# Kernel optimization log

Hardware: AMD Instinct MI355X
Metric: run time of the kernel (lower is better)

Reference implementation:

```python
import jax, jax.numpy as jnp
import numpy as np

B, C, N, K, OUT = 4, 192, 10000, 16, 384

def setup_inputs() -> dict:
    key = jax.random.key(0)
    k1, k2, k3, k4 = jax.random.split(key, 4)
    x = jax.random.normal(k1, (B, C, N, 1), dtype=jnp.float32)
    edge_index = jax.random.randint(k2, (2, B, N, K), 0, N, dtype=jnp.int32)
    # 1x1x1 Conv3d weight [OUT, 2C, 1, 1, 1] collapsed to [OUT, 2C]
    fan_in = 2 * C
    weight = jax.random.normal(k3, (OUT, 2 * C), dtype=jnp.float32) / np.sqrt(fan_in)
    bias = jax.random.normal(k4, (OUT,), dtype=jnp.float32) * 0.01
    return {"x": x, "edge_index": edge_index, "weight": weight, "bias": bias}


def _gather_neighbors(x3, idx):
    # x3: [B, C, N], idx: [B, N, K] -> [B, C, N, K]
    return jax.vmap(lambda xb, ib: xb[:, ib])(x3, idx)


def reference(x, edge_index, weight, bias):
    b, c, n, _ = x.shape
    x3 = x[..., 0]                                   # [B, C, N]
    x_i = _gather_neighbors(x3, edge_index[1])       # centers  [B, C, N, K]
    x_j = _gather_neighbors(x3, edge_index[0])       # neighbors [B, C, N, K]
    x_j_max = jnp.max(x_j - x_i, axis=-1)            # max-relative, [B, C, N]
    # torch.cat([x.unsqueeze(2), x_j.unsqueeze(2)], 2).reshape(b, 2c, n, 1)
    # interleaves channels as (x_c, xj_c) pairs
    feat = jnp.stack([x3, x_j_max], axis=2).reshape(b, 2 * c, n)  # [B, 2C, N]
    out = jnp.einsum('oc,bcn->bon', weight, feat) + bias[None, :, None]
    out = jax.nn.relu(out)
    # Conv3d path: output shape [B, OUT, N, 1, 1]
    return out[..., None, None]
```

## Files before the change

### kernel.cpp

```cpp
#include <hip/hip_runtime.h>
#include <hip/hip_bf16.h>


#define NB   4
#define NC   192
#define NN   10000
#define NK   16
#define NOUT 384
#define K2C  384
#define NPAD 10112

typedef short bf16x8 __attribute__((ext_vector_type(8)));
typedef float f32x4  __attribute__((ext_vector_type(4)));

__device__ inline unsigned short f2bf(float f) {
    unsigned int u = __builtin_bit_cast(unsigned int, f);
    u += ((u >> 16) & 1u) + 0x7FFFu;
    return (unsigned short)(u >> 16);
}
__device__ inline float bflo(unsigned int u) {
    return __builtin_bit_cast(float, u << 16);
}
__device__ inline float bfhi(unsigned int u) {
    return __builtin_bit_cast(float, u & 0xFFFF0000u);
}

__global__ __launch_bounds__(256) void k_transpose(const float* __restrict__ x,
                                                   unsigned short* __restrict__ xT) {
    __shared__ unsigned short tile[NC * 65];
    int b  = blockIdx.x & 3;
    int nb = (blockIdx.x >> 2) * 64;
    int t  = threadIdx.x;
    const float* xb = x + (size_t)b * NC * NN;
    for (int i = 0; i < 48; ++i) {
        int idx = i * 256 + t;
        int c  = idx >> 6;
        int nl = idx & 63;
        int n  = nb + nl;
        float v = (n < NN) ? xb[(size_t)c * NN + n] : 0.f;
        tile[c * 65 + nl] = f2bf(v);
    }
    __syncthreads();
    unsigned short* xTb = xT + (size_t)b * NN * NC;
    for (int i = 0; i < 48; ++i) {
        int idx = i * 256 + t;
        int nl  = idx / NC;
        int c   = idx - nl * NC;
        int n   = nb + nl;
        if (n < NN) xTb[(size_t)n * NC + c] = tile[c * 65 + nl];
    }
}

__global__ __launch_bounds__(256) void k_wconv(const float* __restrict__ w,
                                               unsigned short* __restrict__ wbf) {
    int i = blockIdx.x * 256 + threadIdx.x;
    wbf[i] = f2bf(w[i]);
}

__global__ __launch_bounds__(256, 6) void k_gather(const unsigned short* __restrict__ xT,
                                                   const int* __restrict__ eidx,
                                                   unsigned short* __restrict__ featT) {
    int b    = blockIdx.x & 3;
    int tile = blockIdx.x >> 2;
    int wv   = threadIdx.x >> 6;
    int lane = threadIdx.x & 63;
    int lam  = lane & 31;
    int hb   = lane & 32;
    const unsigned int* xr = (const unsigned int*)(xT + (size_t)b * NN * NC);
    unsigned short* fb = featT + (size_t)b * NPAD * K2C;
    int part = lam >> 4;
    const int* ep = eidx + (size_t)part * NB * NN * NK + (size_t)b * NN * NK;

    int nbase = tile * 64 + wv * 16 + (hb ? 8 : 0);

    int v[8];
#pragma unroll
    for (int it = 0; it < 8; ++it) {
        int n = nbase + it;
        v[it] = (n < NN) ? ep[(size_t)n * NK + (lam & 15)] : 0;
    }

    for (int it = 0; it < 8; ++it) {
        int n = nbase + it;
        if (n >= NN) break;
        const unsigned int* crow = xr + (size_t)n * 96;
        unsigned int c0 = crow[lam], c1 = crow[32 + lam], c2 = crow[64 + lam];
        float m0l = -INFINITY, m0h = -INFINITY;
        float m1l = -INFINITY, m1h = -INFINITY;
        float m2l = -INFINITY, m2h = -INFINITY;
#pragma unroll 4
        for (int k = 0; k < 16; ++k) {
            int j = __shfl(v[it], hb + k, 64);
            int i = __shfl(v[it], hb + 16 + k, 64);
            const unsigned int* rj = xr + (size_t)j * 96;
            const unsigned int* ri = xr + (size_t)i * 96;
            unsigned int j0 = rj[lam], j1 = rj[32 + lam], j2 = rj[64 + lam];
            unsigned int i0 = ri[lam], i1 = ri[32 + lam], i2 = ri[64 + lam];
            m0l = fmaxf(m0l, bflo(j0) - bflo(i0));  m0h = fmaxf(m0h, bfhi(j0) - bfhi(i0));
            m1l = fmaxf(m1l, bflo(j1) - bflo(i1));  m1h = fmaxf(m1h, bfhi(j1) - bfhi(i1));
            m2l = fmaxf(m2l, bflo(j2) - bflo(i2));  m2h = fmaxf(m2h, bfhi(j2) - bfhi(i2));
        }
        uint2* orow = (uint2*)(fb + (size_t)n * K2C);
        uint2 o0, o1, o2;
        o0.x = (c0 & 0xFFFFu)  | ((unsigned int)f2bf(m0l) << 16);
        o0.y = (c0 >> 16)      | ((unsigned int)f2bf(m0h) << 16);
        o1.x = (c1 & 0xFFFFu)  | ((unsigned int)f2bf(m1l) << 16);
        o1.y = (c1 >> 16)      | ((unsigned int)f2bf(m1h) << 16);
        o2.x = (c2 & 0xFFFFu)  | ((unsigned int)f2bf(m2l) << 16);
        o2.y = (c2 >> 16)      | ((unsigned int)f2bf(m2h) << 16);
        orow[lam]      = o0;
        orow[32 + lam] = o1;
        orow[64 + lam] = o2;
    }
}

__global__ __launch_bounds__(256, 3) void k_gemm(const unsigned short* __restrict__ wbf,
                                                 const unsigned short* __restrict__ featT,
                                                 const float* __restrict__ bias,
                                                 float* __restrict__ out) {
    __shared__ unsigned short lds[64 * 48 * 8];
    int bid  = blockIdx.x;
    int b    = bid & 3;
    int nt   = bid >> 2;
    int wv   = threadIdx.x >> 6;
    int lane = threadIdx.x & 63;
    int r    = lane & 15;
    int q    = lane >> 4;

    const unsigned short* fbase = featT + (size_t)b * NPAD * K2C + (size_t)(nt * 64) * K2C;
#pragma unroll
    for (int ii = 0; ii < 12; ++ii) {
        int i = wv * 12 + ii;
        unsigned int g = (unsigned int)(i * 64 + lane);
        unsigned int n = g / 48u;
        unsigned int p = g - n * 48u;
        int j = (int)p - (int)((3u * n) % 48u);
        if (j < 0) j += 48;
        const unsigned short* src = fbase + (size_t)n * K2C + (size_t)j * 8;
        __builtin_amdgcn_global_load_lds(
            (const __attribute__((address_space(1))) unsigned int*)src,
            (__attribute__((address_space(3))) unsigned int*)&lds[(size_t)i * 512],
            16, 0, 0);
    }

    const unsigned short* aptr = wbf + (size_t)(wv * 96 + r) * K2C + q * 8;

    unsigned int nbase[4], u0[4];
#pragma unroll
    for (int ni = 0; ni < 4; ++ni) {
        unsigned int n = ni * 16 + r;
        nbase[ni] = n * 48u;
        u0[ni] = ((unsigned int)q + 3u * n) % 48u;
    }

    f32x4 acc[6][4];
#pragma unroll
    for (int mi = 0; mi < 6; ++mi)
#pragma unroll
        for (int ni = 0; ni < 4; ++ni)
            acc[mi][ni] = (f32x4){0.f, 0.f, 0.f, 0.f};

    __syncthreads();

#pragma unroll 2
    for (int t = 0; t < 12; ++t) {
        bf16x8 a[6], bb[4];
#pragma unroll
        for (int mi = 0; mi < 6; ++mi)
            a[mi] = *(const bf16x8*)(aptr + (size_t)mi * 16 * K2C + t * 32);
#pragma unroll
        for (int ni = 0; ni < 4; ++ni) {
            unsigned int u = u0[ni] + 4u * t;
            if (u >= 48u) u -= 48u;
            bb[ni] = *(const bf16x8*)(lds + (size_t)(nbase[ni] + u) * 8);
        }
#pragma unroll
        for (int mi = 0; mi < 6; ++mi)
#pragma unroll
            for (int ni = 0; ni < 4; ++ni)
                acc[mi][ni] = __builtin_amdgcn_mfma_f32_16x16x32_bf16(a[mi], bb[ni], acc[mi][ni], 0, 0, 0);
    }

    float* ob = out + (size_t)b * NOUT * NN;
#pragma unroll
    for (int mi = 0; mi < 6; ++mi) {
        int obase = wv * 96 + mi * 16 + q * 4;
#pragma unroll
        for (int ni = 0; ni < 4; ++ni) {
            int n = nt * 64 + ni * 16 + r;
            if (n < NN) {
#pragma unroll
                for (int rr = 0; rr < 4; ++rr) {
                    int o = obase + rr;
                    float val = acc[mi][ni][rr] + bias[o];
                    ob[(size_t)o * NN + n] = fmaxf(val, 0.f);
                }
            }
        }
    }
}

extern "C" void kernel_launch(void* const* d_in, const int* in_sizes, int n_in,
                              void* d_out, int out_size, void* d_ws, size_t ws_size,
                              hipStream_t stream) {
    const float* x    = (const float*)d_in[0];
    const int*   eidx = (const int*)d_in[1];
    const float* w    = (const float*)d_in[2];
    const float* bias = (const float*)d_in[3];
    float* out = (float*)d_out;

    unsigned short* xT    = (unsigned short*)d_ws;
    unsigned short* featT = xT + (size_t)NB * NN * NC;
    unsigned short* wbf   = featT + (size_t)NB * NPAD * K2C;

    hipLaunchKernelGGL(k_transpose, dim3(4 * 157), dim3(256), 0, stream, x, xT);
    hipLaunchKernelGGL(k_wconv,     dim3(576),     dim3(256), 0, stream, w, wbf);
    hipLaunchKernelGGL(k_gather,    dim3(4 * 157), dim3(256), 0, stream, xT, eidx, featT);
    hipLaunchKernelGGL(k_gemm,      dim3(4 * 158), dim3(256), 0, stream, wbf, featT, bias, out);
}
```

Baseline: 177.7 us.

## Fuse neighbor gather into GEMM via LDS and merge prep kernels

The gather/max-relative stage now writes its bf16 interleaved feature tile directly into LDS in the swizzled layout the MFMA GEMM expects, so the featT intermediate no longer makes a round trip through global memory and one kernel launch is dropped. The transpose and weight conversion are also merged into one launch, with the weight conversion vectorized to float4. The fused kernel runs at the GEMM's lower occupancy (launch bounds 3 instead of 6), so the latency-bound gather phase has fewer waves to hide its random loads. The GEMM phase also cannot start until the whole tile has been gathered.

```diff
diff --git a/kernel.cpp b/kernel.cpp
--- a/kernel.cpp
+++ b/kernel.cpp
@@ -1,5 +1,4 @@
 #include <hip/hip_runtime.h>
-#include <hip/hip_bf16.h>
 
 
 #define NB   4
@@ -8,7 +7,6 @@
 #define NK   16
 #define NOUT 384
 #define K2C  384
-#define NPAD 10112
 
 typedef short bf16x8 __attribute__((ext_vector_type(8)));
 typedef float f32x4  __attribute__((ext_vector_type(4)));
@@ -25,11 +23,23 @@
     return __builtin_bit_cast(float, u & 0xFFFF0000u);
 }
 
-__global__ __launch_bounds__(256) void k_transpose(const float* __restrict__ x,
-                                                   unsigned short* __restrict__ xT) {
+__global__ __launch_bounds__(256) void k_prep(const float* __restrict__ x,
+                                              unsigned short* __restrict__ xT,
+                                              const float* __restrict__ w,
+                                              unsigned short* __restrict__ wbf) {
     __shared__ unsigned short tile[NC * 65];
-    int b  = blockIdx.x & 3;
-    int nb = (blockIdx.x >> 2) * 64;
+    int bid = blockIdx.x;
+    if (bid >= 628) {
+        int i = (bid - 628) * 256 + threadIdx.x;
+        float4 v = ((const float4*)w)[i];
+        uint2 o;
+        o.x = (unsigned int)f2bf(v.x) | ((unsigned int)f2bf(v.y) << 16);
+        o.y = (unsigned int)f2bf(v.z) | ((unsigned int)f2bf(v.w) << 16);
+        ((uint2*)wbf)[i] = o;
+        return;
+    }
+    int b  = bid & 3;
+    int nb = (bid >> 2) * 64;
     int t  = threadIdx.x;
     const float* xb = x + (size_t)b * NC * NN;
     for (int i = 0; i < 48; ++i) {
@@ -51,38 +61,40 @@
     }
 }
 
-__global__ __launch_bounds__(256) void k_wconv(const float* __restrict__ w,
-                                               unsigned short* __restrict__ wbf) {
-    int i = blockIdx.x * 256 + threadIdx.x;
-    wbf[i] = f2bf(w[i]);
-}
-
-__global__ __launch_bounds__(256, 6) void k_gather(const unsigned short* __restrict__ xT,
-                                                   const int* __restrict__ eidx,
-                                                   unsigned short* __restrict__ featT) {
-    int b    = blockIdx.x & 3;
-    int tile = blockIdx.x >> 2;
+__global__ __launch_bounds__(256, 3) void k_fused(const unsigned short* __restrict__ xT,
+                                                  const int* __restrict__ eidx,
+                                                  const unsigned short* __restrict__ wbf,
+                                                  const float* __restrict__ bias,
+                                                  float* __restrict__ out) {
+    __shared__ unsigned short lds[64 * 48 * 8];
+    int bid  = blockIdx.x;
+    int b    = bid & 3;
+    int nt   = bid >> 2;
     int wv   = threadIdx.x >> 6;
     int lane = threadIdx.x & 63;
     int lam  = lane & 31;
     int hb   = lane & 32;
+    int r    = lane & 15;
+    int q    = lane >> 4;
+
     const unsigned int* xr = (const unsigned int*)(xT + (size_t)b * NN * NC);
-    unsigned short* fb = featT + (size_t)b * NPAD * K2C;
     int part = lam >> 4;
     const int* ep = eidx + (size_t)part * NB * NN * NK + (size_t)b * NN * NK;
-
-    int nbase = tile * 64 + wv * 16 + (hb ? 8 : 0);
+    int nlb = wv * 16 + (hb ? 8 : 0);
+    int gnb = nt * 64 + nlb;
 
     int v[8];
 #pragma unroll
     for (int it = 0; it < 8; ++it) {
-        int n = nbase + it;
+        int n = gnb + it;
         v[it] = (n < NN) ? ep[(size_t)n * NK + (lam & 15)] : 0;
     }
 
+    uint2* l2 = (uint2*)lds;
     for (int it = 0; it < 8; ++it) {
-        int n = nbase + it;
+        int n = gnb + it;
         if (n >= NN) break;
+        int nl = nlb + it;
         const unsigned int* crow = xr + (size_t)n * 96;
         unsigned int c0 = crow[lam], c1 = crow[32 + lam], c2 = crow[64 + lam];
         float m0l = -INFINITY, m0h = -INFINITY;
@@ -100,7 +112,6 @@
             m1l = fmaxf(m1l, bflo(j1) - bflo(i1));  m1h = fmaxf(m1h, bfhi(j1) - bfhi(i1));
             m2l = fmaxf(m2l, bflo(j2) - bflo(i2));  m2h = fmaxf(m2h, bfhi(j2) - bfhi(i2));
         }
-        uint2* orow = (uint2*)(fb + (size_t)n * K2C);
         uint2 o0, o1, o2;
         o0.x = (c0 & 0xFFFFu)  | ((unsigned int)f2bf(m0l) << 16);
         o0.y = (c0 >> 16)      | ((unsigned int)f2bf(m0h) << 16);
@@ -108,40 +119,18 @@
         o1.y = (c1 >> 16)      | ((unsigned int)f2bf(m1h) << 16);
         o2.x = (c2 & 0xFFFFu)  | ((unsigned int)f2bf(m2l) << 16);
         o2.y = (c2 >> 16)      | ((unsigned int)f2bf(m2h) << 16);
-        orow[lam]      = o0;
-        orow[32 + lam] = o1;
-        orow[64 + lam] = o2;
-    }
-}
-
-__global__ __launch_bounds__(256, 3) void k_gemm(const unsigned short* __restrict__ wbf,
-                                                 const unsigned short* __restrict__ featT,
-                                                 const float* __restrict__ bias,
-                                                 float* __restrict__ out) {
-    __shared__ unsigned short lds[64 * 48 * 8];
-    int bid  = blockIdx.x;
-    int b    = bid & 3;
-    int nt   = bid >> 2;
-    int wv   = threadIdx.x >> 6;
-    int lane = threadIdx.x & 63;
-    int r    = lane & 15;
-    int q    = lane >> 4;
-
-    const unsigned short* fbase = featT + (size_t)b * NPAD * K2C + (size_t)(nt * 64) * K2C;
-#pragma unroll
-    for (int ii = 0; ii < 12; ++ii) {
-        int i = wv * 12 + ii;
-        unsigned int g = (unsigned int)(i * 64 + lane);
-        unsigned int n = g / 48u;
-        unsigned int p = g - n * 48u;
-        int j = (int)p - (int)((3u * n) % 48u);
-        if (j < 0) j += 48;
-        const unsigned short* src = fbase + (size_t)n * K2C + (size_t)j * 8;
-        __builtin_amdgcn_global_load_lds(
-            (const __attribute__((address_space(1))) unsigned int*)src,
-            (__attribute__((address_space(3))) unsigned int*)&lds[(size_t)i * 512],
-            16, 0, 0);
-    }
+        unsigned int g  = (unsigned int)(lam >> 1);
+        unsigned int nw = (unsigned int)nl;
+        unsigned int s0 = nw * 48u + (g        + 3u * nw) % 48u;
+        unsigned int s1 = nw * 48u + (g + 16u  + 3u * nw) % 48u;
+        unsigned int s2 = nw * 48u + (g + 32u  + 3u * nw) % 48u;
+        unsigned int half = (unsigned int)(lam & 1);
+        l2[2u * s0 + half] = o0;
+        l2[2u * s1 + half] = o1;
+        l2[2u * s2 + half] = o2;
+    }
+
+    __syncthreads();
 
     const unsigned short* aptr = wbf + (size_t)(wv * 96 + r) * K2C + q * 8;
 
@@ -159,8 +148,6 @@
 #pragma unroll
         for (int ni = 0; ni < 4; ++ni)
             acc[mi][ni] = (f32x4){0.f, 0.f, 0.f, 0.f};
-
-    __syncthreads();
 
 #pragma unroll 2
     for (int t = 0; t < 12; ++t) {
@@ -209,12 +196,9 @@
     const float* bias = (const float*)d_in[3];
     float* out = (float*)d_out;
 
-    unsigned short* xT    = (unsigned short*)d_ws;
-    unsigned short* featT = xT + (size_t)NB * NN * NC;
-    unsigned short* wbf   = featT + (size_t)NB * NPAD * K2C;
-
-    hipLaunchKernelGGL(k_transpose, dim3(4 * 157), dim3(256), 0, stream, x, xT);
-    hipLaunchKernelGGL(k_wconv,     dim3(576),     dim3(256), 0, stream, w, wbf);
-    hipLaunchKernelGGL(k_gather,    dim3(4 * 157), dim3(256), 0, stream, xT, eidx, featT);
-    hipLaunchKernelGGL(k_gemm,      dim3(4 * 158), dim3(256), 0, stream, wbf, featT, bias, out);
-}
+    unsigned short* xT  = (unsigned short*)d_ws;
+    unsigned short* wbf = xT + (size_t)NB * NN * NC;
+
+    hipLaunchKernelGGL(k_prep,  dim3(628 + 144), dim3(256), 0, stream, x, xT, w, wbf);
+    hipLaunchKernelGGL(k_fused, dim3(4 * 157),   dim3(256), 0, stream, xT, eidx, wbf, bias, out);
+}
```

Result: faster. 167.3 us (-5.8%).
